# Kernel optimization log

Hardware: AMD Instinct MI355X
Metric: run time of the kernel (lower is better)

The kernel has to match this reference:

```python
import jax, jax.numpy as jnp
import numpy as np

LAYERS = 8
HID = 512
IN_F = 6
OUT_F = 3
N = 131072
# forward factors as computed by MipNet.forward from default factors [(0.5,0.5),(1,0.5),(1,1)]
FACTORS = [(0.5, 0.5, 0.0, 0.0), (1.0, 0.5, 0.5, 0.5), (1.0, 1.0, 1.0, 0.5)]
EPS = 1e-5


def _lin(x, W, b, f, sf):
    # slice sub-weight per factor f, with stop_gradient on the sub-subfactor block
    r = int(round(W.shape[0] * f[0]))
    c = int(round(W.shape[1] * f[1]))
    r2 = int(round(W.shape[0] * sf[0]))
    c2 = int(round(W.shape[1] * sf[1]))
    mw = jnp.concatenate([jax.lax.stop_gradient(W[:r2, :c2]), W[:r2, c2:c]], axis=1)
    mw = jnp.concatenate([mw, W[r2:r, :c]], axis=0)
    mb = jnp.concatenate([jax.lax.stop_gradient(b[:r2]), b[r2:r]])
    return x @ mw.T + mb[None]


def _ln(x, w, b, f, sf):
    mean = jnp.mean(x, axis=1, keepdims=True)
    var = jnp.mean((x - mean) ** 2, axis=1, keepdims=True)  # unbiased=False
    xn = (x - mean) / jnp.sqrt(var + EPS)
    s = int(round(w.shape[0] * f))
    s2 = int(round(w.shape[0] * sf))
    sw = jnp.concatenate([jax.lax.stop_gradient(w[:s2]), w[s2:s]])
    sb = jnp.concatenate([jax.lax.stop_gradient(b[:s2]), b[s2:s]])
    return sw[None] * xn + sb[None]


def setup_inputs() -> dict:
    key = jax.random.key(0)
    ks = jax.random.split(key, 8)
    return {
        "inputs": jax.random.normal(ks[0], (N, IN_F), dtype=jnp.float32),
        "W_in": jax.random.normal(ks[1], (HID, IN_F), dtype=jnp.float32) * 0.05,
        "b_in": jax.random.normal(ks[2], (HID,), dtype=jnp.float32) * 0.05,
        "Ws": jax.random.normal(ks[3], (LAYERS - 2, HID, HID), dtype=jnp.float32) * 0.05,
        "bs": jax.random.normal(ks[4], (LAYERS - 2, HID), dtype=jnp.float32) * 0.05,
        "ln_w": jnp.ones((LAYERS - 1, HID), dtype=jnp.float32),
        "ln_b": jnp.zeros((LAYERS - 1, HID), dtype=jnp.float32),
        "W_out": jax.random.normal(ks[5], (OUT_F, HID), dtype=jnp.float32) * 0.05,
        "b_out": jax.random.normal(ks[6], (OUT_F,), dtype=jnp.float32) * 0.05,
    }


def reference(inputs, W_in, b_in, Ws, bs, ln_w, ln_b, W_out, b_out):
    outs = []
    for f in FACTORS:
        x = _lin(inputs, W_in, b_in, (f[0], 1.0), (f[2], 1.0))
        x = _ln(x, ln_w[0], ln_b[0], f[0], f[2])
        x = jax.nn.relu(x)
        for i in range(1, LAYERS - 1):
            mf = (f[i % 2], f[(i + 1) % 2])
            msf = (f[2 + i % 2], f[2 + (i + 1) % 2])
            x = _lin(x, Ws[i - 1], bs[i - 1], mf, msf)
            x = _ln(x, ln_w[i], ln_b[i], mf[0], msf[0])
            x = jax.nn.relu(x)
        x = _lin(x, W_out, b_out, (1.0, f[LAYERS % 2]), (1.0, f[2 + LAYERS % 2]))
        outs.append(x)
    return jnp.stack(outs, axis=1)  # [N, num_factors, OUT_F]
```

## Files before the change

### kernel.cpp

```cpp
#include <hip/hip_runtime.h>

typedef _Float16 f16;
typedef _Float16 f16x8 __attribute__((ext_vector_type(8)));
typedef float f32x16 __attribute__((ext_vector_type(16)));
typedef unsigned short u16;
typedef unsigned int u32;

#define NSAMP 131072
#define HID 512
#define NW 8
#define ST 4
#define BSAMP 128

#define ACT_BYTES (BSAMP * 1024)
#define STATS_OFF ACT_BYTES
#define LDS_TOTAL (ACT_BYTES + NW * BSAMP * 8)

__host__ __device__ constexpr int wact(int f, int l) {
    if (f == 0) return 256;
    if (f == 2) return 512;
    return (l & 1) ? 256 : 512;
}
__host__ __device__ constexpr int seg_tiles(int f, int l) {
    if (l == 0) return wact(f, 0) / 32;
    if (l == 7) return wact(f, 6) / 16;
    return (wact(f, l) / 32) * (wact(f, l - 1) / 16);
}
__host__ __device__ constexpr int seg_off(int f, int l) {
    int o = 0;
    for (int ff = 0; ff < 3; ++ff)
        for (int ll = 0; ll < 8; ++ll) {
            if (ff == f && ll == l) return o;
            o += seg_tiles(ff, ll);
        }
    return o;
}
constexpr int TOTAL_TILES = seg_off(2, 7) + seg_tiles(2, 7);

__global__ __launch_bounds__(256) void prep_kernel(const float* __restrict__ W_in,
                                                   const float* __restrict__ Ws,
                                                   const float* __restrict__ W_out,
                                                   u16* __restrict__ wt) {
    int b = blockIdx.x;
    int f = 0, l = 0, start = 0;
    for (int s = 0; s < 24; ++s) {
        int ff = s >> 3, ll = s & 7;
        int t = seg_tiles(ff, ll);
        if (b < start + t) { f = ff; l = ll; break; }
        start += t;
    }
    int lt = b - start;
    int FT = (l == 7) ? 1 : wact(f, l) / 32;
    int sh = (FT == 16) ? 4 : (FT == 8) ? 3 : 0;
    int kt = lt >> sh;
    int ft = lt & (FT - 1);
    const float* src; int stride, vr, vc;
    if (l == 0)      { src = W_in;                     stride = 6;   vr = 512; vc = 6;   }
    else if (l == 7) { src = W_out;                    stride = HID; vr = 3;   vc = HID; }
    else             { src = Ws + (l - 1) * HID * HID; stride = HID; vr = HID; vc = HID; }
    u16* dst = wt + (size_t)b * 512;
    #pragma unroll
    for (int t = 0; t < 2; ++t) {
        int e = threadIdx.x * 2 + t;
        int lane = e >> 3, j = e & 7;
        int row = ft * 32 + (lane & 31);
        int col = kt * 16 + (lane >> 5) * 8 + j;
        float v = (row < vr && col < vc) ? src[row * stride + col] : 0.0f;
        dst[e] = __builtin_bit_cast(u16, (f16)v);
    }
}

__device__ __forceinline__ f32x16 zero16() {
    f32x16 z = {0.f,0.f,0.f,0.f,0.f,0.f,0.f,0.f,0.f,0.f,0.f,0.f,0.f,0.f,0.f,0.f};
    return z;
}
__device__ __forceinline__ f16x8 bc(const uint4 v) { return __builtin_bit_cast(f16x8, v); }

template<int FW, int DOUT>
__device__ __forceinline__ void epilogue(f32x16 (&acc)[FW][ST],
                                         const float* __restrict__ bias,
                                         const float* __restrict__ lw,
                                         const float* __restrict__ lb,
                                         char* act, char* stats,
                                         int ft0, int w, int sl, int h, int swz) {
    constexpr float invD = 1.0f / DOUT;
    float s[ST] = {0.f,0.f,0.f,0.f}, ss[ST] = {0.f,0.f,0.f,0.f};
    #pragma unroll
    for (int j = 0; j < FW; ++j) {
        #pragma unroll
        for (int q = 0; q < 4; ++q) {
            float4 bv = *reinterpret_cast<const float4*>(bias + (ft0 + j) * 32 + q * 8 + h * 4);
            #pragma unroll
            for (int st = 0; st < ST; ++st) {
                #pragma unroll
                for (int r = 0; r < 4; ++r) {
                    float v = acc[j][st][q * 4 + r] + (&bv.x)[r];
                    acc[j][st][q * 4 + r] = v;
                    s[st] += v; ss[st] += v * v;
                }
            }
        }
    }
    #pragma unroll
    for (int st = 0; st < ST; ++st) {
        s[st]  += __shfl_xor(s[st], 32);
        ss[st] += __shfl_xor(ss[st], 32);
    }
    if (h == 0) {
        #pragma unroll
        for (int st = 0; st < ST; ++st)
            *reinterpret_cast<float2*>(stats + ((size_t)w * BSAMP + st * 32 + sl) * 8) =
                make_float2(s[st], ss[st]);
    }
    __syncthreads();
    float mean_[ST], rstd_[ST];
    #pragma unroll
    for (int st = 0; st < ST; ++st) {
        float S = 0.f, SS = 0.f;
        #pragma unroll
        for (int ww = 0; ww < NW; ++ww) {
            float2 p = *reinterpret_cast<const float2*>(stats + ((size_t)ww * BSAMP + st * 32 + sl) * 8);
            S += p.x; SS += p.y;
        }
        float mean = S * invD;
        float var  = SS * invD - mean * mean;
        mean_[st] = mean;
        rstd_[st] = 1.0f / sqrtf(var + 1e-5f);
    }
    #pragma unroll
    for (int j = 0; j < FW; ++j) {
        #pragma unroll
        for (int q = 0; q < 4; ++q) {
            float4 wv  = *reinterpret_cast<const float4*>(lw + (ft0 + j) * 32 + q * 8 + h * 4);
            float4 lbv = *reinterpret_cast<const float4*>(lb + (ft0 + j) * 32 + q * 8 + h * 4);
            #pragma unroll
            for (int st = 0; st < ST; ++st) {
                float o[4];
                #pragma unroll
                for (int r = 0; r < 4; ++r) {
                    f16 x16 = (f16)acc[j][st][q * 4 + r];
                    float xn = (((float)x16) - mean_[st]) * rstd_[st];
                    o[r] = fmaxf((&wv.x)[r] * xn + (&lbv.x)[r], 0.f);
                }
                u32 p0 = (u32)__builtin_bit_cast(u16, (f16)o[0]) | ((u32)__builtin_bit_cast(u16, (f16)o[1]) << 16);
                u32 p1 = (u32)__builtin_bit_cast(u16, (f16)o[2]) | ((u32)__builtin_bit_cast(u16, (f16)o[3]) << 16);
                int byte = (st * 32 + sl) * 1024 + (((ft0 + j) * 64 + q * 16 + h * 8) ^ swz);
                *reinterpret_cast<uint2*>(act + byte) = make_uint2(p0, p1);
            }
        }
    }
    __syncthreads();
}

template<int DIN, int DOUT>
__device__ __forceinline__ void hidden(const u16* __restrict__ seg,
                                       const float* __restrict__ bias,
                                       const float* __restrict__ lw,
                                       const float* __restrict__ lb,
                                       char* act, char* stats,
                                       int w, int lane, int h, int sl, int swz) {
    constexpr int KT = DIN / 16, FTT = DOUT / 32, FW = FTT / NW;
    constexpr int AST = FTT * 1024;
    const int ft0 = w * FW;
    f32x16 acc[FW][ST];
    #pragma unroll
    for (int j = 0; j < FW; ++j)
        #pragma unroll
        for (int st = 0; st < ST; ++st) acc[j][st] = zero16();
    const char* abase = (const char*)seg + (size_t)ft0 * 1024 + lane * 16;
    uint4 cur[FW], nxt[FW];
    #pragma unroll
    for (int j = 0; j < FW; ++j) cur[j] = *reinterpret_cast<const uint4*>(abase + j * 1024);
    #pragma unroll
    for (int j = 0; j < FW; ++j) nxt[j] = *reinterpret_cast<const uint4*>(abase + AST + j * 1024);
    #pragma unroll 2
    for (int kt = 0; kt < KT; ++kt) {
        uint4 pf[FW];
        const int ktp = (kt + 2 < KT) ? (kt + 2) : kt;
        #pragma unroll
        for (int j = 0; j < FW; ++j)
            pf[j] = *reinterpret_cast<const uint4*>(abase + (size_t)ktp * AST + j * 1024);
        f16x8 B[ST];
        #pragma unroll
        for (int st = 0; st < ST; ++st)
            B[st] = bc(*reinterpret_cast<const uint4*>(act + (st * 32 + sl) * 1024 + ((kt * 32 + h * 16) ^ swz)));
        #pragma unroll
        for (int j = 0; j < FW; ++j) {
            f16x8 A = bc(cur[j]);
            #pragma unroll
            for (int st = 0; st < ST; ++st)
                acc[j][st] = __builtin_amdgcn_mfma_f32_32x32x16_f16(A, B[st], acc[j][st], 0, 0, 0);
        }
        #pragma unroll
        for (int j = 0; j < FW; ++j) { cur[j] = nxt[j]; nxt[j] = pf[j]; }
    }
    epilogue<FW, DOUT>(acc, bias, lw, lb, act, stats, ft0, w, sl, h, swz);
}

template<int DOUT>
__device__ __forceinline__ void layer_in(const u16* __restrict__ seg,
                                         const float* __restrict__ bias,
                                         const float* __restrict__ lw,
                                         const float* __restrict__ lb,
                                         char* act, char* stats, const f16x8 (&ib)[ST],
                                         int w, int lane, int h, int sl, int swz) {
    constexpr int FTT = DOUT / 32, FW = FTT / NW;
    const int ft0 = w * FW;
    f32x16 acc[FW][ST];
    #pragma unroll
    for (int j = 0; j < FW; ++j)
        #pragma unroll
        for (int st = 0; st < ST; ++st) acc[j][st] = zero16();
    const char* abase = (const char*)seg + (size_t)ft0 * 1024 + lane * 16;
    #pragma unroll
    for (int j = 0; j < FW; ++j) {
        f16x8 A = bc(*reinterpret_cast<const uint4*>(abase + j * 1024));
        #pragma unroll
        for (int st = 0; st < ST; ++st)
            acc[j][st] = __builtin_amdgcn_mfma_f32_32x32x16_f16(A, ib[st], acc[j][st], 0, 0, 0);
    }
    epilogue<FW, DOUT>(acc, bias, lw, lb, act, stats, ft0, w, sl, h, swz);
}

template<int DIN>
__device__ __forceinline__ void layer_out(const u16* __restrict__ seg,
                                          const float* __restrict__ b_out,
                                          const char* act, float* __restrict__ out,
                                          int F, int samp0, int w, int lane, int h, int sl, int swz) {
    if (w < ST) {
        constexpr int KT = DIN / 16;
        f32x16 acc = zero16();
        const char* abase = (const char*)seg + lane * 16;
        const int samp = w * 32 + sl;
        #pragma unroll
        for (int kt = 0; kt < KT; ++kt) {
            f16x8 A = bc(*reinterpret_cast<const uint4*>(abase + kt * 1024));
            f16x8 B = bc(*reinterpret_cast<const uint4*>(act + samp * 1024 + ((kt * 32 + h * 16) ^ swz)));
            acc = __builtin_amdgcn_mfma_f32_32x32x16_f16(A, B, acc, 0, 0, 0);
        }
        if (h == 0) {
            float* o = out + (size_t)(samp0 + samp) * 9 + F * 3;
            o[0] = acc[0] + b_out[0];
            o[1] = acc[1] + b_out[1];
            o[2] = acc[2] + b_out[2];
        }
    }
}

template<int F>
__device__ __forceinline__ void run_factor(const float* __restrict__ b_in,
                                           const float* __restrict__ bs,
                                           const float* __restrict__ lnw,
                                           const float* __restrict__ lnb,
                                           const float* __restrict__ b_out,
                                           const u16* __restrict__ wt,
                                           float* __restrict__ out,
                                           char* act, char* stats, const f16x8 (&ib)[ST],
                                           int samp0, int w, int lane, int h, int sl, int swz) {
    layer_in<wact(F,0)>(wt + (size_t)seg_off(F,0) * 512, b_in, lnw, lnb, act, stats, ib, w, lane, h, sl, swz);
    hidden<wact(F,0), wact(F,1)>(wt + (size_t)seg_off(F,1) * 512, bs + 0*HID, lnw + 1*HID, lnb + 1*HID, act, stats, w, lane, h, sl, swz);
    hidden<wact(F,1), wact(F,2)>(wt + (size_t)seg_off(F,2) * 512, bs + 1*HID, lnw + 2*HID, lnb + 2*HID, act, stats, w, lane, h, sl, swz);
    hidden<wact(F,2), wact(F,3)>(wt + (size_t)seg_off(F,3) * 512, bs + 2*HID, lnw + 3*HID, lnb + 3*HID, act, stats, w, lane, h, sl, swz);
    hidden<wact(F,3), wact(F,4)>(wt + (size_t)seg_off(F,4) * 512, bs + 3*HID, lnw + 4*HID, lnb + 4*HID, act, stats, w, lane, h, sl, swz);
    hidden<wact(F,4), wact(F,5)>(wt + (size_t)seg_off(F,5) * 512, bs + 4*HID, lnw + 5*HID, lnb + 5*HID, act, stats, w, lane, h, sl, swz);
    hidden<wact(F,5), wact(F,6)>(wt + (size_t)seg_off(F,6) * 512, bs + 5*HID, lnw + 6*HID, lnb + 6*HID, act, stats, w, lane, h, sl, swz);
    layer_out<wact(F,6)>(wt + (size_t)seg_off(F,7) * 512, b_out, act, out, F, samp0, w, lane, h, sl, swz);
}

__global__ __launch_bounds__(NW * 64, 2) void mipnet_kernel(
        const float* __restrict__ inp, const float* __restrict__ b_in,
        const float* __restrict__ bs, const float* __restrict__ lnw,
        const float* __restrict__ lnb, const float* __restrict__ b_out,
        const u16* __restrict__ wt, float* __restrict__ out) {
    extern __shared__ char lds[];
    char* act   = lds;
    char* stats = lds + STATS_OFF;
    const int tid  = threadIdx.x;
    const int w    = tid >> 6;
    const int lane = tid & 63;
    const int h    = lane >> 5;
    const int sl   = lane & 31;
    const int swz  = (sl & 15) << 4;
    const int samp0 = blockIdx.x * BSAMP;

    f16x8 ib[ST];
    #pragma unroll
    for (int st = 0; st < ST; ++st) {
        f16x8 B = {(f16)0.f,(f16)0.f,(f16)0.f,(f16)0.f,(f16)0.f,(f16)0.f,(f16)0.f,(f16)0.f};
        if (h == 0) {
            const float* p = inp + (size_t)(samp0 + st * 32 + sl) * 6;
            float2 v0 = *reinterpret_cast<const float2*>(p + 0);
            float2 v1 = *reinterpret_cast<const float2*>(p + 2);
            float2 v2 = *reinterpret_cast<const float2*>(p + 4);
            B[0] = (f16)v0.x; B[1] = (f16)v0.y;
            B[2] = (f16)v1.x; B[3] = (f16)v1.y;
            B[4] = (f16)v2.x; B[5] = (f16)v2.y;
        }
        ib[st] = B;
    }
    run_factor<0>(b_in, bs, lnw, lnb, b_out, wt, out, act, stats, ib, samp0, w, lane, h, sl, swz);
    run_factor<1>(b_in, bs, lnw, lnb, b_out, wt, out, act, stats, ib, samp0, w, lane, h, sl, swz);
    run_factor<2>(b_in, bs, lnw, lnb, b_out, wt, out, act, stats, ib, samp0, w, lane, h, sl, swz);
}

extern "C" void kernel_launch(void* const* d_in, const int* in_sizes, int n_in,
                              void* d_out, int out_size, void* d_ws, size_t ws_size,
                              hipStream_t stream) {
    (void)in_sizes; (void)n_in; (void)out_size; (void)ws_size;
    const float* inputs = (const float*)d_in[0];
    const float* W_in   = (const float*)d_in[1];
    const float* b_in   = (const float*)d_in[2];
    const float* Ws     = (const float*)d_in[3];
    const float* bs     = (const float*)d_in[4];
    const float* lnw    = (const float*)d_in[5];
    const float* lnb    = (const float*)d_in[6];
    const float* W_out  = (const float*)d_in[7];
    const float* b_out  = (const float*)d_in[8];
    u16* wt = (u16*)d_ws;

    hipFuncSetAttribute(reinterpret_cast<const void*>(mipnet_kernel),
                        hipFuncAttributeMaxDynamicSharedMemorySize, LDS_TOTAL);

    prep_kernel<<<TOTAL_TILES, 256, 0, stream>>>(W_in, Ws, W_out, wt);
    mipnet_kernel<<<NSAMP / BSAMP, NW * 64, LDS_TOTAL, stream>>>(
        inputs, b_in, bs, lnw, lnb, b_out, wt, (float*)d_out);
}
```

Baseline: 1.356 ms.

## Halve sample block, raise occupancy, packed-f16 LayerNorm epilogue, shallower prefetch

```diff
diff --git a/kernel.cpp b/kernel.cpp
--- a/kernel.cpp
+++ b/kernel.cpp
@@ -1,6 +1,7 @@
 #include <hip/hip_runtime.h>
 
 typedef _Float16 f16;
+typedef _Float16 f16x2 __attribute__((ext_vector_type(2)));
 typedef _Float16 f16x8 __attribute__((ext_vector_type(8)));
 typedef float f32x16 __attribute__((ext_vector_type(16)));
 typedef unsigned short u16;
@@ -9,8 +10,8 @@
 #define NSAMP 131072
 #define HID 512
 #define NW 8
-#define ST 4
-#define BSAMP 128
+#define ST 2
+#define BSAMP 64
 
 #define ACT_BYTES (BSAMP * 1024)
 #define STATS_OFF ACT_BYTES
@@ -36,12 +37,27 @@
     return o;
 }
 constexpr int TOTAL_TILES = seg_off(2, 7) + seg_tiles(2, 7);
+#define LTAB_OFF ((size_t)TOTAL_TILES * 512)
 
 __global__ __launch_bounds__(256) void prep_kernel(const float* __restrict__ W_in,
                                                    const float* __restrict__ Ws,
                                                    const float* __restrict__ W_out,
+                                                   const float* __restrict__ lnw,
+                                                   const float* __restrict__ lnb,
                                                    u16* __restrict__ wt) {
     int b = blockIdx.x;
+    if (b >= TOTAL_TILES) {
+        int l = b - TOTAL_TILES;
+        int t = threadIdx.x;
+        u16* dst = wt + LTAB_OFF + (size_t)l * 1024;
+        const float* src = (t < 128) ? (lnw + l * HID) : (lnb + l * HID);
+        int base = (t < 128) ? t * 4 : (t - 128) * 4;
+        int dbase = (t < 128) ? t * 4 : 512 + (t - 128) * 4;
+        #pragma unroll
+        for (int k = 0; k < 4; ++k)
+            dst[dbase + k] = __builtin_bit_cast(u16, (f16)src[base + k]);
+        return;
+    }
     int f = 0, l = 0, start = 0;
     for (int s = 0; s < 24; ++s) {
         int ff = s >> 3, ll = s & 7;
@@ -75,16 +91,21 @@
     return z;
 }
 __device__ __forceinline__ f16x8 bc(const uint4 v) { return __builtin_bit_cast(f16x8, v); }
+__device__ __forceinline__ f16x2 bc2(const u32 v) { return __builtin_bit_cast(f16x2, v); }
+__device__ __forceinline__ f16x2 pkrtz(float a, float b) {
+    return __builtin_bit_cast(f16x2, __builtin_amdgcn_cvt_pkrtz(a, b));
+}
 
 template<int FW, int DOUT>
 __device__ __forceinline__ void epilogue(f32x16 (&acc)[FW][ST],
                                          const float* __restrict__ bias,
-                                         const float* __restrict__ lw,
-                                         const float* __restrict__ lb,
+                                         const u16* __restrict__ lt,
                                          char* act, char* stats,
                                          int ft0, int w, int sl, int h, int swz) {
     constexpr float invD = 1.0f / DOUT;
-    float s[ST] = {0.f,0.f,0.f,0.f}, ss[ST] = {0.f,0.f,0.f,0.f};
+    float s[ST], ss[ST];
+    #pragma unroll
+    for (int st = 0; st < ST; ++st) { s[st] = 0.f; ss[st] = 0.f; }
     #pragma unroll
     for (int j = 0; j < FW; ++j) {
         #pragma unroll
@@ -113,7 +134,7 @@
                 make_float2(s[st], ss[st]);
     }
     __syncthreads();
-    float mean_[ST], rstd_[ST];
+    f16x2 r2a[ST], c2a[ST];
     #pragma unroll
     for (int st = 0; st < ST; ++st) {
         float S = 0.f, SS = 0.f;
@@ -124,28 +145,33 @@
         }
         float mean = S * invD;
         float var  = SS * invD - mean * mean;
-        mean_[st] = mean;
-        rstd_[st] = 1.0f / sqrtf(var + 1e-5f);
-    }
+        float rstd = 1.0f / sqrtf(var + 1e-5f);
+        f16 r16 = (f16)rstd;
+        f16 c16 = (f16)(-mean * rstd);
+        r2a[st] = f16x2{r16, r16};
+        c2a[st] = f16x2{c16, c16};
+    }
+    const f16x2 zz = f16x2{(f16)0.f, (f16)0.f};
     #pragma unroll
     for (int j = 0; j < FW; ++j) {
         #pragma unroll
         for (int q = 0; q < 4; ++q) {
-            float4 wv  = *reinterpret_cast<const float4*>(lw + (ft0 + j) * 32 + q * 8 + h * 4);
-            float4 lbv = *reinterpret_cast<const float4*>(lb + (ft0 + j) * 32 + q * 8 + h * 4);
+            const int f = (ft0 + j) * 32 + q * 8 + h * 4;
+            uint2 lwu = *reinterpret_cast<const uint2*>(lt + f);
+            uint2 lbu = *reinterpret_cast<const uint2*>(lt + 512 + f);
+            f16x2 lw0 = bc2(lwu.x), lw1 = bc2(lwu.y);
+            f16x2 lb0 = bc2(lbu.x), lb1 = bc2(lbu.y);
             #pragma unroll
             for (int st = 0; st < ST; ++st) {
-                float o[4];
-                #pragma unroll
-                for (int r = 0; r < 4; ++r) {
-                    f16 x16 = (f16)acc[j][st][q * 4 + r];
-                    float xn = (((float)x16) - mean_[st]) * rstd_[st];
-                    o[r] = fmaxf((&wv.x)[r] * xn + (&lbv.x)[r], 0.f);
-                }
-                u32 p0 = (u32)__builtin_bit_cast(u16, (f16)o[0]) | ((u32)__builtin_bit_cast(u16, (f16)o[1]) << 16);
-                u32 p1 = (u32)__builtin_bit_cast(u16, (f16)o[2]) | ((u32)__builtin_bit_cast(u16, (f16)o[3]) << 16);
-                int byte = (st * 32 + sl) * 1024 + (((ft0 + j) * 64 + q * 16 + h * 8) ^ swz);
-                *reinterpret_cast<uint2*>(act + byte) = make_uint2(p0, p1);
+                f16x2 x0 = pkrtz(acc[j][st][q*4+0], acc[j][st][q*4+1]);
+                f16x2 x1 = pkrtz(acc[j][st][q*4+2], acc[j][st][q*4+3]);
+                f16x2 xn0 = __builtin_elementwise_fma(x0, r2a[st], c2a[st]);
+                f16x2 xn1 = __builtin_elementwise_fma(x1, r2a[st], c2a[st]);
+                f16x2 y0 = __builtin_elementwise_max(__builtin_elementwise_fma(lw0, xn0, lb0), zz);
+                f16x2 y1 = __builtin_elementwise_max(__builtin_elementwise_fma(lw1, xn1, lb1), zz);
+                int byte = (st * 32 + sl) * 1024 + ((f * 2) ^ swz);
+                *reinterpret_cast<uint2*>(act + byte) =
+                    make_uint2(__builtin_bit_cast(u32, y0), __builtin_bit_cast(u32, y1));
             }
         }
     }
@@ -155,8 +181,7 @@
 template<int DIN, int DOUT>
 __device__ __forceinline__ void hidden(const u16* __restrict__ seg,
                                        const float* __restrict__ bias,
-                                       const float* __restrict__ lw,
-                                       const float* __restrict__ lb,
+                                       const u16* __restrict__ lt,
                                        char* act, char* stats,
                                        int w, int lane, int h, int sl, int swz) {
     constexpr int KT = DIN / 16, FTT = DOUT / 32, FW = FTT / NW;
@@ -171,15 +196,12 @@
     uint4 cur[FW], nxt[FW];
     #pragma unroll
     for (int j = 0; j < FW; ++j) cur[j] = *reinterpret_cast<const uint4*>(abase + j * 1024);
-    #pragma unroll
-    for (int j = 0; j < FW; ++j) nxt[j] = *reinterpret_cast<const uint4*>(abase + AST + j * 1024);
     #pragma unroll 2
     for (int kt = 0; kt < KT; ++kt) {
-        uint4 pf[FW];
-        const int ktp = (kt + 2 < KT) ? (kt + 2) : kt;
+        const int ktn = (kt + 1 < KT) ? (kt + 1) : kt;
         #pragma unroll
         for (int j = 0; j < FW; ++j)
-            pf[j] = *reinterpret_cast<const uint4*>(abase + (size_t)ktp * AST + j * 1024);
+            nxt[j] = *reinterpret_cast<const uint4*>(abase + (size_t)ktn * AST + j * 1024);
         f16x8 B[ST];
         #pragma unroll
         for (int st = 0; st < ST; ++st)
@@ -192,16 +214,15 @@
                 acc[j][st] = __builtin_amdgcn_mfma_f32_32x32x16_f16(A, B[st], acc[j][st], 0, 0, 0);
         }
         #pragma unroll
-        for (int j = 0; j < FW; ++j) { cur[j] = nxt[j]; nxt[j] = pf[j]; }
-    }
-    epilogue<FW, DOUT>(acc, bias, lw, lb, act, stats, ft0, w, sl, h, swz);
+        for (int j = 0; j < FW; ++j) cur[j] = nxt[j];
+    }
+    epilogue<FW, DOUT>(acc, bias, lt, act, stats, ft0, w, sl, h, swz);
 }
 
 template<int DOUT>
 __device__ __forceinline__ void layer_in(const u16* __restrict__ seg,
                                          const float* __restrict__ bias,
-                                         const float* __restrict__ lw,
-                                         const float* __restrict__ lb,
+                                         const u16* __restrict__ lt,
                                          char* act, char* stats, const f16x8 (&ib)[ST],
                                          int w, int lane, int h, int sl, int swz) {
     constexpr int FTT = DOUT / 32, FW = FTT / NW;
@@ -219,7 +240,7 @@
         for (int st = 0; st < ST; ++st)
             acc[j][st] = __builtin_amdgcn_mfma_f32_32x32x16_f16(A, ib[st], acc[j][st], 0, 0, 0);
     }
-    epilogue<FW, DOUT>(acc, bias, lw, lb, act, stats, ft0, w, sl, h, swz);
+    epilogue<FW, DOUT>(acc, bias, lt, act, stats, ft0, w, sl, h, swz);
 }
 
 template<int DIN>
@@ -250,27 +271,25 @@
 template<int F>
 __device__ __forceinline__ void run_factor(const float* __restrict__ b_in,
                                            const float* __restrict__ bs,
-                                           const float* __restrict__ lnw,
-                                           const float* __restrict__ lnb,
                                            const float* __restrict__ b_out,
                                            const u16* __restrict__ wt,
                                            float* __restrict__ out,
                                            char* act, char* stats, const f16x8 (&ib)[ST],
                                            int samp0, int w, int lane, int h, int sl, int swz) {
-    layer_in<wact(F,0)>(wt + (size_t)seg_off(F,0) * 512, b_in, lnw, lnb, act, stats, ib, w, lane, h, sl, swz);
-    hidden<wact(F,0), wact(F,1)>(wt + (size_t)seg_off(F,1) * 512, bs + 0*HID, lnw + 1*HID, lnb + 1*HID, act, stats, w, lane, h, sl, swz);
-    hidden<wact(F,1), wact(F,2)>(wt + (size_t)seg_off(F,2) * 512, bs + 1*HID, lnw + 2*HID, lnb + 2*HID, act, stats, w, lane, h, sl, swz);
-    hidden<wact(F,2), wact(F,3)>(wt + (size_t)seg_off(F,3) * 512, bs + 2*HID, lnw + 3*HID, lnb + 3*HID, act, stats, w, lane, h, sl, swz);
-    hidden<wact(F,3), wact(F,4)>(wt + (size_t)seg_off(F,4) * 512, bs + 3*HID, lnw + 4*HID, lnb + 4*HID, act, stats, w, lane, h, sl, swz);
-    hidden<wact(F,4), wact(F,5)>(wt + (size_t)seg_off(F,5) * 512, bs + 4*HID, lnw + 5*HID, lnb + 5*HID, act, stats, w, lane, h, sl, swz);
-    hidden<wact(F,5), wact(F,6)>(wt + (size_t)seg_off(F,6) * 512, bs + 5*HID, lnw + 6*HID, lnb + 6*HID, act, stats, w, lane, h, sl, swz);
+    const u16* ltab = wt + LTAB_OFF;
+    layer_in<wact(F,0)>(wt + (size_t)seg_off(F,0) * 512, b_in, ltab, act, stats, ib, w, lane, h, sl, swz);
+    hidden<wact(F,0), wact(F,1)>(wt + (size_t)seg_off(F,1) * 512, bs + 0*HID, ltab + 1*1024, act, stats, w, lane, h, sl, swz);
+    hidden<wact(F,1), wact(F,2)>(wt + (size_t)seg_off(F,2) * 512, bs + 1*HID, ltab + 2*1024, act, stats, w, lane, h, sl, swz);
+    hidden<wact(F,2), wact(F,3)>(wt + (size_t)seg_off(F,3) * 512, bs + 2*HID, ltab + 3*1024, act, stats, w, lane, h, sl, swz);
+    hidden<wact(F,3), wact(F,4)>(wt + (size_t)seg_off(F,4) * 512, bs + 3*HID, ltab + 4*1024, act, stats, w, lane, h, sl, swz);
+    hidden<wact(F,4), wact(F,5)>(wt + (size_t)seg_off(F,5) * 512, bs + 4*HID, ltab + 5*1024, act, stats, w, lane, h, sl, swz);
+    hidden<wact(F,5), wact(F,6)>(wt + (size_t)seg_off(F,6) * 512, bs + 5*HID, ltab + 6*1024, act, stats, w, lane, h, sl, swz);
     layer_out<wact(F,6)>(wt + (size_t)seg_off(F,7) * 512, b_out, act, out, F, samp0, w, lane, h, sl, swz);
 }
 
-__global__ __launch_bounds__(NW * 64, 2) void mipnet_kernel(
+__global__ __launch_bounds__(NW * 64, 4) void mipnet_kernel(
         const float* __restrict__ inp, const float* __restrict__ b_in,
-        const float* __restrict__ bs, const float* __restrict__ lnw,
-        const float* __restrict__ lnb, const float* __restrict__ b_out,
+        const float* __restrict__ bs, const float* __restrict__ b_out,
         const u16* __restrict__ wt, float* __restrict__ out) {
     extern __shared__ char lds[];
     char* act   = lds;
@@ -298,9 +317,9 @@
         }
         ib[st] = B;
     }
-    run_factor<0>(b_in, bs, lnw, lnb, b_out, wt, out, act, stats, ib, samp0, w, lane, h, sl, swz);
-    run_factor<1>(b_in, bs, lnw, lnb, b_out, wt, out, act, stats, ib, samp0, w, lane, h, sl, swz);
-    run_factor<2>(b_in, bs, lnw, lnb, b_out, wt, out, act, stats, ib, samp0, w, lane, h, sl, swz);
+    run_factor<0>(b_in, bs, b_out, wt, out, act, stats, ib, samp0, w, lane, h, sl, swz);
+    run_factor<1>(b_in, bs, b_out, wt, out, act, stats, ib, samp0, w, lane, h, sl, swz);
+    run_factor<2>(b_in, bs, b_out, wt, out, act, stats, ib, samp0, w, lane, h, sl, swz);
 }
 
 extern "C" void kernel_launch(void* const* d_in, const int* in_sizes, int n_in,
@@ -321,7 +340,7 @@
     hipFuncSetAttribute(reinterpret_cast<const void*>(mipnet_kernel),
                         hipFuncAttributeMaxDynamicSharedMemorySize, LDS_TOTAL);
 
-    prep_kernel<<<TOTAL_TILES, 256, 0, stream>>>(W_in, Ws, W_out, wt);
+    prep_kernel<<<TOTAL_TILES + 7, 256, 0, stream>>>(W_in, Ws, W_out, lnw, lnb, wt);
     mipnet_kernel<<<NSAMP / BSAMP, NW * 64, LDS_TOTAL, stream>>>(
-        inputs, b_in, bs, lnw, lnb, b_out, wt, (float*)d_out);
-}
+        inputs, b_in, bs, b_out, wt, (float*)d_out);
+}
```

Result: slower. 1.470 ms (+8.4%).
